# Optimization experiments

Hardware: AMD Instinct MI355X
Metric: run time of the kernel (lower is better)

Reference implementation:

```python
import jax, jax.numpy as jnp
from jax import lax
import numpy as np

B, DIM, HEADS, L, K = 8, 128, 8, 4096, 3
INNER = DIM * HEADS
PAD = K // 2
EPS = 1e-5
SCALE = DIM ** -0.5


def setup_inputs() -> dict:
    key = jax.random.key(0)
    ks = jax.random.split(key, 32)

    def n(i, shape, s):
        return jax.random.normal(ks[i], shape, jnp.float32) * s

    inp = {"x": jax.random.normal(ks[0], (B, DIM, L), jnp.float32)}
    inp["ln1_g"] = jnp.ones((DIM,), jnp.float32)
    inp["ln1_b"] = jnp.zeros((DIM,), jnp.float32)
    for idx, p in enumerate(("q", "k", "v")):
        base = 1 + idx * 2
        inp[p + "_dw"] = n(base, (DIM, 1, K), 0.2)        # depthwise kernel
        inp[p + "_bn_g"] = jnp.ones((DIM,), jnp.float32)
        inp[p + "_bn_b"] = jnp.zeros((DIM,), jnp.float32)
        inp[p + "_bn_m"] = jnp.zeros((DIM,), jnp.float32)  # running mean
        inp[p + "_bn_v"] = jnp.ones((DIM,), jnp.float32)   # running var
        inp[p + "_pw"] = n(base + 1, (INNER, DIM), 0.05)   # 1x1 conv dim->inner
    inp["dwc_dw"] = n(8, (DIM,), 0.2)                      # kernel-1 depthwise = per-channel scale
    inp["dwc_bn_g"] = jnp.ones((DIM,), jnp.float32)
    inp["dwc_bn_b"] = jnp.zeros((DIM,), jnp.float32)
    inp["dwc_bn_m"] = jnp.zeros((DIM,), jnp.float32)
    inp["dwc_bn_v"] = jnp.ones((DIM,), jnp.float32)
    inp["dwc_pw"] = n(9, (DIM, DIM), 0.05)
    inp["out_w"] = n(10, (DIM, INNER), 0.05)
    inp["out_b"] = jnp.zeros((DIM,), jnp.float32)
    inp["ln2_g"] = jnp.ones((DIM,), jnp.float32)
    inp["ln2_b"] = jnp.zeros((DIM,), jnp.float32)
    inp["ff_w1"] = n(11, (4 * DIM, DIM), 0.05)
    inp["ff_b1"] = jnp.zeros((4 * DIM,), jnp.float32)
    inp["ff_w2"] = n(12, (DIM, 4 * DIM), 0.05)
    inp["ff_b2"] = jnp.zeros((DIM,), jnp.float32)
    return inp


def _layernorm(x, g, b):
    # channel-wise LN over axis=1 (unbiased=False variance)
    m = jnp.mean(x, axis=1, keepdims=True)
    v = jnp.var(x, axis=1, keepdims=True)
    return (x - m) / jnp.sqrt(v + EPS) * g[None, :, None] + b[None, :, None]


def _dw_block(x, dw, g, b, m, v, pw):
    # depthwise conv (k=K, same padding) -> eval-mode BN -> 1x1 conv
    y = lax.conv_general_dilated(x, dw, (1,), [(PAD, PAD)],
                                 feature_group_count=DIM,
                                 dimension_numbers=("NCH", "OIH", "NCH"))
    y = (y - m[None, :, None]) * (g / jnp.sqrt(v + EPS))[None, :, None] + b[None, :, None]
    return jnp.einsum("oi,bil->bol", pw, y)


def reference(x, ln1_g, ln1_b,
              q_dw, q_bn_g, q_bn_b, q_bn_m, q_bn_v, q_pw,
              k_dw, k_bn_g, k_bn_b, k_bn_m, k_bn_v, k_pw,
              v_dw, v_bn_g, v_bn_b, v_bn_m, v_bn_v, v_pw,
              dwc_dw, dwc_bn_g, dwc_bn_b, dwc_bn_m, dwc_bn_v, dwc_pw,
              out_w, out_b, ln2_g, ln2_b, ff_w1, ff_b1, ff_w2, ff_b2):
    # ---- attention block (PreNorm + residual) ----
    xn = _layernorm(x, ln1_g, ln1_b)
    q = _dw_block(xn, q_dw, q_bn_g, q_bn_b, q_bn_m, q_bn_v, q_pw)  # [B, INNER, L]
    k = _dw_block(xn, k_dw, k_bn_g, k_bn_b, k_bn_m, k_bn_v, k_pw)
    v = _dw_block(xn, v_dw, v_bn_g, v_bn_b, v_bn_m, v_bn_v, v_pw)

    def split(t):  # b (h d) x -> (b h) x d
        return t.reshape(B, HEADS, DIM, L).transpose(0, 1, 3, 2).reshape(B * HEADS, L, DIM)

    q, k, v = split(q), split(k), split(v)
    k_soft = jax.nn.softmax(k, axis=-1)                       # softmax over feature dim d
    kk = jnp.einsum("nxd,nxe->nde", q, k_soft) * SCALE        # [(bh), d, d]
    # DWConv gate on q (kernel-1 depthwise -> BN -> 1x1), channels = DIM
    g_ = q * dwc_dw[None, None, :]
    g_ = (g_ - dwc_bn_m) * (dwc_bn_g / jnp.sqrt(dwc_bn_v + EPS)) + dwc_bn_b
    g_ = jnp.einsum("od,nxd->nxo", dwc_pw, g_)
    gate = jax.nn.sigmoid(g_) * v
    out = jnp.einsum("nxd,nde->nxe", v, kk) + gate            # [(bh), L, d]
    out = out.reshape(B, HEADS, L, DIM).transpose(0, 1, 3, 2).reshape(B, INNER, L)
    attn = jnp.einsum("oi,bil->bol", out_w, out) + out_b[None, :, None]
    x = attn + x

    # ---- feed-forward block (PreNorm + residual) ----
    xn = _layernorm(x, ln2_g, ln2_b)
    h = jnp.einsum("oi,bil->bol", ff_w1, xn) + ff_b1[None, :, None]
    h = jax.nn.gelu(h, approximate=False)
    h = jnp.einsum("oi,bil->bol", ff_w2, h) + ff_b2[None, :, None]
    return h + x
```

## Files before the change

### kernel.cpp

```cpp
#include <hip/hip_runtime.h>
#include <hip/hip_bf16.h>
#include <math.h>

#define DI __device__ __forceinline__

namespace {

constexpr int L = 4096;
constexpr float EPS = 1e-5f;
constexpr float SCALEF = 0.08838834764831845f;

typedef unsigned short u16;
typedef unsigned int u32;
typedef unsigned char u8;
typedef __attribute__((ext_vector_type(8))) short bf16x8;
typedef __attribute__((ext_vector_type(4))) float f32x4;

DI float b2f(u16 h){ u32 u = ((u32)h) << 16; float f; __builtin_memcpy(&f, &u, 4); return f; }
DI u16 f2b(float f){ u32 u; __builtin_memcpy(&u, &f, 4); u32 r = u + 0x7fffu + ((u >> 16) & 1u); return (u16)(r >> 16); }
DI float sigmoidf(float x){ return 1.f / (1.f + __expf(-x)); }

DI uint2 pack_fp8x8(const float* v){
  u32 lo = __builtin_amdgcn_cvt_pk_fp8_f32(v[0], v[1], 0, false);
  lo = (u32)__builtin_amdgcn_cvt_pk_fp8_f32(v[2], v[3], lo, true);
  u32 hi = __builtin_amdgcn_cvt_pk_fp8_f32(v[4], v[5], 0, false);
  hi = (u32)__builtin_amdgcn_cvt_pk_fp8_f32(v[6], v[7], hi, true);
  return make_uint2(lo, hi);
}
DI u8 f2e(float v){ return (u8)__builtin_amdgcn_cvt_pk_fp8_f32(v, v, 0, false); }
DI float e2f(u8 c){ return __builtin_amdgcn_cvt_f32_fp8((int)c, 0); }

DI int boff(int o, int d8){ return ((o >> 4) << 11) + (d8 << 7) + (((o & 15) ^ d8) << 3); }
DI int foff(int g, int k8, int nn){ return (g << 11) + (k8 << 7) + (nn << 3); }
DI int faddr(int x, int e){ return ((x >> 4) << 11) + ((e >> 3) << 7) + ((x & 15) << 3) + (e & 7); }
DI int t8off(int dhi, int nl, int x8){ return (dhi << 11) + (x8 << 7) + (((nl ^ x8 ^ dhi) & 15) << 3); }

DI void stage_a(const u16* __restrict__ g, int rs, u16* a_s, int tid){
  #pragma unroll
  for (int it = 0; it < 4; it++){
    int item = tid + 256 * it;
    int d8 = item & 15, l = item >> 4;
    *(uint4*)&a_s[l * 136 + d8 * 8] = *(const uint4*)&g[(size_t)l * rs + d8 * 8];
  }
}

__global__ __launch_bounds__(256) void ln_kernel(
    const float* __restrict__ x, const float* __restrict__ g,
    const float* __restrict__ bt, u16* __restrict__ o)
{
  const int tid = threadIdx.x;
  const int pos = blockIdx.x * 64 + (tid >> 2);
  const int part = tid & 3;
  const int b = pos >> 12, l = pos & (L - 1);
  const float* xb = x + (size_t)b * 128 * L + l;
  float vv[32];
  float s = 0.f, ss = 0.f;
  #pragma unroll
  for (int i = 0; i < 32; i++){
    float v = xb[(size_t)(part * 32 + i) * L];
    vv[i] = v; s += v; ss += v * v;
  }
  s += __shfl_xor(s, 1);  s += __shfl_xor(s, 2);
  ss += __shfl_xor(ss, 1); ss += __shfl_xor(ss, 2);
  const float m = s * (1.f / 128.f);
  const float rs = rsqrtf(ss * (1.f / 128.f) - m * m + EPS);
  #pragma unroll
  for (int c = 0; c < 4; c++){
    u16 pk[8];
    #pragma unroll
    for (int j = 0; j < 8; j++){
      int d = part * 32 + c * 8 + j;
      pk[j] = f2b((vv[c * 8 + j] - m) * rs * g[d] + bt[d]);
    }
    uint4 uu; __builtin_memcpy(&uu, pk, 16);
    *(uint4*)&o[(size_t)pos * 128 + part * 32 + c * 8] = uu;
  }
}

__global__ __launch_bounds__(256) void wpack_kernel(
    const float* __restrict__ q_pw, const float* __restrict__ k_pw,
    const float* __restrict__ v_pw, const float* __restrict__ out_w,
    const float* __restrict__ ff_w1, const float* __restrict__ ff_w2,
    const float* __restrict__ dwc_dw, const float* __restrict__ dwc_bng,
    const float* __restrict__ dwc_bnv, const float* __restrict__ dwc_bnb,
    const float* __restrict__ dwc_bnm, const float* __restrict__ dwc_pw,
    u16* __restrict__ wpk, float* __restrict__ c2, u8* __restrict__ wpk8)
{
  const int blk = blockIdx.x;
  const int tid = threadIdx.x;
  if (blk < 37){
    int t8 = blk;
    #pragma unroll
    for (int it = 0; it < 8; it++){
      int item = tid + 256 * it;
      int nn = item & 15, k8 = (item >> 4) & 15, os = item >> 8;
      int o = os * 16 + nn;
      float fv[8];
      if (t8 < 24){
        int p = t8 >> 3, h = t8 & 7;
        const float* pw = (p == 0) ? q_pw : (p == 1 ? k_pw : v_pw);
        #pragma unroll
        for (int j = 0; j < 8; j++)
          fv[j] = pw[(size_t)(h * 128 + o) * 128 + k8 * 8 + j] * 16.f;
      } else if (t8 < 32){
        #pragma unroll
        for (int j = 0; j < 8; j++)
          fv[j] = out_w[(size_t)o * 1024 + (t8 - 24) * 128 + k8 * 8 + j] * 16.f;
      } else if (t8 < 36){
        #pragma unroll
        for (int j = 0; j < 8; j++)
          fv[j] = ff_w1[(size_t)((t8 - 32) * 128 + o) * 128 + k8 * 8 + j] * 16.f;
      } else {
        #pragma unroll
        for (int j = 0; j < 8; j++){
          int d = k8 * 8 + j;
          float sD = dwc_bng[d] * rsqrtf(dwc_bnv[d] + EPS);
          fv[j] = dwc_pw[(size_t)o * 128 + d] * dwc_dw[d] * sD * 16.f;
        }
      }
      *(uint2*)&wpk8[(size_t)t8 * 16384 + foff(os, k8, nn)] = pack_fp8x8(fv);
    }
  } else if (blk < 69){
    int vitem = (blk - 37) * 256 + tid;
    int d8 = vitem & 15;
    int o  = (vitem >> 4) & 127;
    int t  = 36 + (vitem >> 11);
    const float* src = ff_w2 + (size_t)o * 512 + (t - 36) * 128 + d8 * 8;
    u16 pk[8];
    #pragma unroll
    for (int j = 0; j < 8; j++) pk[j] = f2b(src[j]);
    uint4 uu; __builtin_memcpy(&uu, pk, 16);
    *(uint4*)&wpk[(size_t)t * 16384 + boff(o, d8)] = uu;
  } else {
    int e = tid;
    if (e < 128){
      float cacc = 0.f;
      for (int d = 0; d < 128; d++){
        float sD = dwc_bng[d] * rsqrtf(dwc_bnv[d] + EPS);
        cacc += dwc_pw[(size_t)e * 128 + d] * (dwc_bnb[d] - dwc_bnm[d] * sD);
      }
      c2[e] = cacc;
    }
  }
}

struct QkvArgs {
  const float* dw[3];
  const float* bng[3];
  const float* bnb[3];
  const float* bnm[3];
  const float* bnv[3];
  u8* outp[3];
};

__global__ __launch_bounds__(256, 5) void qkv_fused_kernel(
    const u16* __restrict__ xnb, const u8* __restrict__ wpk8, QkvArgs args)
{
  __shared__ __attribute__((aligned(16))) u8 y_s8[64 * 136];
  __shared__ __attribute__((aligned(16))) u8 w_s8[16384];
  __shared__ float4 coef[128];
  const int tid = threadIdx.x;
  const int lb = blockIdx.x;
  const int bz = blockIdx.y;
  const int b  = bz / 3;
  const int p  = bz % 3;
  const int l0 = lb * 64;
  const int lane = tid & 63, wv = tid >> 6;
  const int nn = lane & 15, quad = lane >> 4;
  const int d8s = tid & 15;

  if (tid < 128){
    int d = tid;
    float sD = args.bng[p][d] * rsqrtf(args.bnv[p][d] + EPS);
    const float* dw = args.dw[p];
    coef[d] = make_float4(dw[d * 3] * sD, dw[d * 3 + 1] * sD, dw[d * 3 + 2] * sD,
                          args.bnb[p][d] - args.bnm[p][d] * sD);
  }
  __syncthreads();
  float4 cf[8];
  #pragma unroll
  for (int jj = 0; jj < 8; jj++) cf[jj] = coef[d8s * 8 + jj];
  #pragma unroll
  for (int it = 0; it < 4; it++){
    int l = (tid >> 4) + it * 16;
    int gl = l0 + l;
    const u16* rowp = xnb + ((size_t)b * L + gl) * 128 + d8s * 8;
    uint4 uc = *(const uint4*)rowp;
    uint4 um = (gl > 0)     ? *(const uint4*)(rowp - 128) : make_uint4(0, 0, 0, 0);
    uint4 up = (gl < L - 1) ? *(const uint4*)(rowp + 128) : make_uint4(0, 0, 0, 0);
    u16 em[8], ec[8], ep[8];
    __builtin_memcpy(em, &um, 16); __builtin_memcpy(ec, &uc, 16); __builtin_memcpy(ep, &up, 16);
    float fv[8];
    #pragma unroll
    for (int jj = 0; jj < 8; jj++)
      fv[jj] = cf[jj].x * b2f(em[jj]) + cf[jj].y * b2f(ec[jj]) + cf[jj].z * b2f(ep[jj]) + cf[jj].w;
    *(uint2*)&y_s8[l * 136 + d8s * 8] = pack_fp8x8(fv);
  }
  __syncthreads();
  long afq[4];
  #pragma unroll
  for (int dc = 0; dc < 4; dc++)
    afq[dc] = *(const long*)&y_s8[(wv * 16 + nn) * 136 + ((dc << 2) + quad) * 8];

  for (int h = 0; h < 8; h++){
    if (h) __syncthreads();
    const u8* src = wpk8 + ((size_t)(p * 8 + h) << 14);
    #pragma unroll
    for (int it = 0; it < 4; it++){
      int idx = (tid + 256 * it) << 4;
      *(uint4*)&w_s8[idx] = *(const uint4*)&src[idx];
    }
    __syncthreads();
    f32x4 acc[8];
    #pragma unroll
    for (int os = 0; os < 8; os++) acc[os] = (f32x4){0.f, 0.f, 0.f, 0.f};
    #pragma unroll
    for (int os = 0; os < 8; os++){
      #pragma unroll
      for (int dc = 0; dc < 4; dc++){
        int d8 = (dc << 2) + quad;
        long bf8 = *(const long*)&w_s8[foff(os, d8, nn)];
        acc[os] = __builtin_amdgcn_mfma_f32_16x16x32_fp8_fp8(afq[dc], bf8, acc[os], 0, 0, 0);
      }
    }
    #pragma unroll
    for (int os = 0; os < 8; os++)
      #pragma unroll
      for (int r = 0; r < 4; r++) acc[os][r] *= 0.0625f;
    if (p == 1){
      #pragma unroll
      for (int r = 0; r < 4; r++){
        float m = acc[0][r];
        #pragma unroll
        for (int os = 1; os < 8; os++) m = fmaxf(m, acc[os][r]);
        m = fmaxf(m, __shfl_xor(m, 1));
        m = fmaxf(m, __shfl_xor(m, 2));
        m = fmaxf(m, __shfl_xor(m, 4));
        m = fmaxf(m, __shfl_xor(m, 8));
        float s = 0.f;
        #pragma unroll
        for (int os = 0; os < 8; os++){ acc[os][r] = __expf(acc[os][r] - m); s += acc[os][r]; }
        s += __shfl_xor(s, 1);
        s += __shfl_xor(s, 2);
        s += __shfl_xor(s, 4);
        s += __shfl_xor(s, 8);
        float inv = 16.f / s;
        #pragma unroll
        for (int os = 0; os < 8; os++) acc[os][r] *= inv;
      }
    }
    __syncthreads();
    u8* st8 = w_s8;
    if (p == 2){
      #pragma unroll
      for (int os = 0; os < 8; os++){
        int e = (os << 4) + nn;
        #pragma unroll
        for (int r = 0; r < 4; r++)
          st8[faddr(wv * 16 + quad * 4 + r, e)] = f2e(acc[os][r]);
      }
    } else {
      #pragma unroll
      for (int os = 0; os < 8; os++){
        int e = (os << 4) + nn;
        #pragma unroll
        for (int r = 0; r < 4; r++)
          st8[(wv * 16 + quad * 4 + r) * 136 + e] = f2e(acc[os][r]);
      }
    }
    __syncthreads();
    if (p == 2){
      u8* v8 = args.outp[2];
      size_t tbase = ((size_t)((b * 8 + h) * 64 + lb)) << 13;
      #pragma unroll
      for (int it = 0; it < 2; it++){
        int idx = (tid + 256 * it) << 4;
        *(uint4*)&v8[tbase + idx] = *(const uint4*)&st8[idx];
      }
    } else {
      u8* outp8 = args.outp[p];
      size_t gbase = ((size_t)(b * 8 + h) * L + l0) * 128;
      #pragma unroll
      for (int it = 0; it < 4; it++){
        int item = tid + 256 * it;
        int row = item >> 4, d8 = item & 15;
        *(uint2*)&outp8[gbase + (size_t)row * 128 + d8 * 8] =
            *(const uint2*)&st8[row * 136 + d8 * 8];
      }
    }
  }
}

__global__ __launch_bounds__(256, 3) void kk_kernel(
    const u8* __restrict__ qt8, const u8* __restrict__ kt8,
    float* __restrict__ kkp)
{
  __shared__ u8 qT8[16384];
  __shared__ u8 kT8[16384];
  const int tid = threadIdx.x;
  const int sp = blockIdx.x;
  const int n  = blockIdx.y;
  const int d8 = tid & 15;
  const int x8 = tid >> 4;
  const int lane = tid & 63, wv = tid >> 6;
  const int nn = lane & 15, quad = lane >> 4;
  const int m4 = (wv >> 1) << 2;
  const int e4 = (wv & 1) << 2;
  const size_t gbase = ((size_t)n * L + sp * 1024) * 128;

  uint2 rq[8], rk[8];
  #pragma unroll
  for (int j = 0; j < 8; j++){
    size_t off = gbase + (size_t)(x8 * 8 + j) * 128 + d8 * 8;
    rq[j] = *(const uint2*)&qt8[off];
    rk[j] = *(const uint2*)&kt8[off];
  }

  f32x4 acc[4][4];
  #pragma unroll
  for (int mi = 0; mi < 4; mi++)
    #pragma unroll
    for (int ei = 0; ei < 4; ei++) acc[mi][ei] = (f32x4){0.f, 0.f, 0.f, 0.f};

  for (int c = 0; c < 8; c++){
    #pragma unroll
    for (int i = 0; i < 8; i++){
      u8 cq[8], ck[8];
      #pragma unroll
      for (int j = 0; j < 8; j++){
        u8 tmp[8];
        __builtin_memcpy(tmp, &rq[j], 8); cq[j] = tmp[i];
        __builtin_memcpy(tmp, &rk[j], 8); ck[j] = tmp[i];
      }
      int d = d8 * 8 + i;
      int off = t8off(d >> 4, d & 15, x8);
      uint2 uq, uk;
      __builtin_memcpy(&uq, cq, 8); __builtin_memcpy(&uk, ck, 8);
      *(uint2*)&qT8[off] = uq;
      *(uint2*)&kT8[off] = uk;
    }
    __syncthreads();
    if (c < 7){
      #pragma unroll
      for (int j = 0; j < 8; j++){
        size_t off = gbase + (size_t)((c + 1) * 128 + x8 * 8 + j) * 128 + d8 * 8;
        rq[j] = *(const uint2*)&qt8[off];
        rk[j] = *(const uint2*)&kt8[off];
      }
    }
    #pragma unroll
    for (int ks = 0; ks < 4; ks++){
      int x8f = (ks << 2) + quad;
      long af[4], bf[4];
      #pragma unroll
      for (int t = 0; t < 4; t++){
        af[t] = *(const long*)&qT8[t8off(m4 + t, nn, x8f)];
        bf[t] = *(const long*)&kT8[t8off(e4 + t, nn, x8f)];
      }
      #pragma unroll
      for (int mi = 0; mi < 4; mi++)
        #pragma unroll
        for (int ei = 0; ei < 4; ei++)
          acc[mi][ei] = __builtin_amdgcn_mfma_f32_16x16x32_fp8_fp8(af[mi], bf[ei], acc[mi][ei], 0, 0, 0);
    }
    __syncthreads();
  }

  float* op = kkp + ((size_t)(sp * 64 + n) << 14);
  #pragma unroll
  for (int mi = 0; mi < 4; mi++){
    #pragma unroll
    for (int r = 0; r < 4; r++){
      int d = (m4 << 4) + mi * 16 + quad * 4 + r;
      #pragma unroll
      for (int ei = 0; ei < 4; ei++)
        op[d * 128 + (e4 << 4) + ei * 16 + nn] = acc[mi][ei][r];
    }
  }
}

__global__ __launch_bounds__(256) void kkred_kernel(
    const float* __restrict__ kkp, u8* __restrict__ kkbb8)
{
  int item = blockIdx.x * 256 + threadIdx.x;
  int nn = item & 15, d8 = (item >> 4) & 15, os = (item >> 8) & 7, n = item >> 11;
  int e = os * 16 + nn;
  float fv[8];
  #pragma unroll
  for (int j = 0; j < 8; j++){
    float s = 0.f;
    #pragma unroll
    for (int sp = 0; sp < 4; sp++)
      s += kkp[(size_t)sp * (64 * 16384) + n * 16384 + (d8 * 8 + j) * 128 + e];
    fv[j] = s * (SCALEF * 2.f);
  }
  *(uint2*)&kkbb8[((size_t)n << 14) + foff(os, d8, nn)] = pack_fp8x8(fv);
}

__global__ __launch_bounds__(256, 4) void gateout_kernel(
    const u8* __restrict__ qt8, const u8* __restrict__ vt8,
    const u8* __restrict__ kkbb8, const u8* __restrict__ w2tb8,
    const float* __restrict__ c2, u8* __restrict__ outt8)
{
  __shared__ __attribute__((aligned(16))) u8 q_s8[64 * 144];
  __shared__ __attribute__((aligned(16))) u8 v_s8[8192];
  const int tid = threadIdx.x;
  const int lb = blockIdx.x;
  const int n  = blockIdx.y;
  const int l0 = lb * 64;
  const int lane = tid & 63, wv = tid >> 6;
  const int nn = lane & 15, quad = lane >> 4;
  const size_t vtile = ((size_t)(n * 64 + lb)) << 13;
  const size_t qbase = ((size_t)n * L + l0) * 128;

  #pragma unroll
  for (int it = 0; it < 4; it++){
    int item = tid + 256 * it;
    int d8b = item & 15, l = item >> 4;
    *(uint2*)&q_s8[l * 144 + d8b * 8] = *(const uint2*)&qt8[qbase + (size_t)l * 128 + d8b * 8];
  }
  #pragma unroll
  for (int it = 0; it < 2; it++){
    int idx = (tid + 256 * it) << 4;
    *(uint4*)&v_s8[idx] = *(const uint4*)&vt8[vtile + idx];
  }
  __syncthreads();

  long aq[4], av[4];
  #pragma unroll
  for (int dc = 0; dc < 4; dc++){
    aq[dc] = *(const long*)&q_s8[(wv * 16 + nn) * 144 + ((dc << 2) + quad) * 8];
    av[dc] = *(const long*)&v_s8[foff(wv, (dc << 2) + quad, nn)];
  }
  const u8* kb8 = kkbb8 + ((size_t)n << 14);
  f32x4 acc_o[8], acc_g[8];
  #pragma unroll
  for (int os = 0; os < 8; os++){ acc_o[os] = (f32x4){0,0,0,0}; acc_g[os] = (f32x4){0,0,0,0}; }
  #pragma unroll
  for (int os = 0; os < 8; os++){
    #pragma unroll
    for (int dc = 0; dc < 4; dc++){
      int d8 = (dc << 2) + quad;
      long bkk = *(const long*)&kb8[foff(os, d8, nn)];
      long bw8 = *(const long*)&w2tb8[foff(os, d8, nn)];
      acc_o[os] = __builtin_amdgcn_mfma_f32_16x16x32_fp8_fp8(av[dc], bkk, acc_o[os], 0, 0, 0);
      acc_g[os] = __builtin_amdgcn_mfma_f32_16x16x32_fp8_fp8(aq[dc], bw8, acc_g[os], 0, 0, 0);
    }
  }
  __syncthreads();
  u8* st8 = q_s8;
  #pragma unroll
  for (int os = 0; os < 8; os++){
    int e = (os << 4) + nn;
    float c2v = c2[e];
    #pragma unroll
    for (int r = 0; r < 4; r++){
      int xr = wv * 16 + quad * 4 + r;
      float ve = e2f(v_s8[faddr(xr, e)]);
      float val = acc_o[os][r] * (1.f / 32.f) + sigmoidf(acc_g[os][r] * 0.0625f + c2v) * ve;
      st8[faddr(xr, e)] = f2e(val);
    }
  }
  __syncthreads();
  #pragma unroll
  for (int it = 0; it < 2; it++){
    int idx = (tid + 256 * it) << 4;
    *(uint4*)&outt8[vtile + idx] = *(const uint4*)&st8[idx];
  }
}

__global__ __launch_bounds__(256, 4) void outw_kernel(
    const u8* __restrict__ outt8, const u8* __restrict__ wpk8o,
    const float* __restrict__ out_b, const float* __restrict__ x,
    const float* __restrict__ g2, const float* __restrict__ bt2,
    float* __restrict__ x2, u8* __restrict__ xn2b8)
{
  __shared__ float stf[128 * 68];
  const int tid = threadIdx.x;
  const int lb = blockIdx.x;
  const int b  = blockIdx.y;
  const int l0 = lb * 64;
  const int lane = tid & 63, wv = tid >> 6;
  const int nn = lane & 15, quad = lane >> 4;
  f32x4 acc[8];
  #pragma unroll
  for (int os = 0; os < 8; os++) acc[os] = (f32x4){0,0,0,0};

  for (int h = 0; h < 8; h++){
    const size_t tbase = ((size_t)((b * 8 + h) * 64 + lb)) << 13;
    long af[4];
    #pragma unroll
    for (int dc = 0; dc < 4; dc++)
      af[dc] = *(const long*)&outt8[tbase + foff(wv, (dc << 2) + quad, nn)];
    const u8* bp8 = wpk8o + (h << 14);
    #pragma unroll
    for (int os = 0; os < 8; os++){
      #pragma unroll
      for (int dc = 0; dc < 4; dc++){
        long bf8 = *(const long*)&bp8[foff(os, (dc << 2) + quad, nn)];
        acc[os] = __builtin_amdgcn_mfma_f32_16x16x32_fp8_fp8(af[dc], bf8, acc[os], 0, 0, 0);
      }
    }
  }
  #pragma unroll
  for (int os = 0; os < 8; os++)
    #pragma unroll
    for (int r = 0; r < 4; r++)
      stf[((os << 4) + nn) * 68 + wv * 16 + quad * 4 + r] = acc[os][r] * 0.0625f;
  __syncthreads();
  {
    int o = tid >> 1, lh = tid & 1;
    float bias = out_b[o];
    size_t gbase = ((size_t)b * 128 + o) * L + l0 + lh * 32;
    float* sp = &stf[o * 68 + lh * 32];
    #pragma unroll
    for (int k = 0; k < 8; k++){
      float4 xv = *(const float4*)&x[gbase + k * 4];
      float4 sv = *(float4*)&sp[k * 4];
      float4 ov = make_float4(sv.x + bias + xv.x, sv.y + bias + xv.y,
                              sv.z + bias + xv.z, sv.w + bias + xv.w);
      *(float4*)&sp[k * 4] = ov;
      *(float4*)&x2[gbase + k * 4] = ov;
    }
  }
  __syncthreads();
  {
    int l = tid >> 2, part = tid & 3;
    float vv[32];
    float s = 0.f, ss = 0.f;
    #pragma unroll
    for (int i = 0; i < 32; i++){
      float v = stf[(part * 32 + i) * 68 + l];
      vv[i] = v; s += v; ss += v * v;
    }
    s += __shfl_xor(s, 1);  s += __shfl_xor(s, 2);
    ss += __shfl_xor(ss, 1); ss += __shfl_xor(ss, 2);
    float m = s * (1.f / 128.f);
    float rs = rsqrtf(ss * (1.f / 128.f) - m * m + EPS);
    #pragma unroll
    for (int c = 0; c < 4; c++){
      float fv[8];
      #pragma unroll
      for (int j = 0; j < 8; j++){
        int d = part * 32 + c * 8 + j;
        fv[j] = (vv[c * 8 + j] - m) * rs * g2[d] + bt2[d];
      }
      *(uint2*)&xn2b8[((size_t)b * L + l0 + l) * 128 + part * 32 + c * 8] = pack_fp8x8(fv);
    }
  }
}

__global__ __launch_bounds__(256, 4) void ff_fused_kernel(
    const u8* __restrict__ xn2b8, const u8* __restrict__ wpk8,
    const u16* __restrict__ wpk,
    const float* __restrict__ b1, const float* __restrict__ b2,
    const float* __restrict__ x2, float* __restrict__ outp)
{
  __shared__ __attribute__((aligned(16))) u8 a_s8[64 * 136];
  __shared__ u16 h_s[64 * 136];
  const int tid = threadIdx.x;
  const int lb = blockIdx.x;
  const int b  = blockIdx.y;
  const int l0 = lb * 64;
  const int lane = tid & 63, wv = tid >> 6;
  const int nn = lane & 15, quad = lane >> 4;

  #pragma unroll
  for (int it = 0; it < 4; it++){
    int item = tid + 256 * it;
    int d8 = item & 15, l = item >> 4;
    *(uint2*)&a_s8[l * 136 + d8 * 8] =
        *(const uint2*)&xn2b8[((size_t)b * L + l0 + l) * 128 + d8 * 8];
  }
  __syncthreads();
  long af8[4];
  #pragma unroll
  for (int dc = 0; dc < 4; dc++)
    af8[dc] = *(const long*)&a_s8[(wv * 16 + nn) * 136 + ((dc << 2) + quad) * 8];

  f32x4 acc_out[8];
  #pragma unroll
  for (int os = 0; os < 8; os++) acc_out[os] = (f32x4){0.f, 0.f, 0.f, 0.f};

  for (int fc = 0; fc < 4; fc++){
    const u8* bp1 = wpk8 + (size_t)(32 + fc) * 16384;
    f32x4 hacc[8];
    #pragma unroll
    for (int os = 0; os < 8; os++) hacc[os] = (f32x4){0.f, 0.f, 0.f, 0.f};
    #pragma unroll
    for (int os = 0; os < 8; os++){
      #pragma unroll
      for (int dc = 0; dc < 4; dc++){
        long bf8 = *(const long*)&bp1[foff(os, (dc << 2) + quad, nn)];
        hacc[os] = __builtin_amdgcn_mfma_f32_16x16x32_fp8_fp8(af8[dc], bf8, hacc[os], 0, 0, 0);
      }
    }
    __syncthreads();
    #pragma unroll
    for (int os = 0; os < 8; os++){
      float bias = b1[fc * 128 + (os << 4) + nn];
      #pragma unroll
      for (int r = 0; r < 4; r++){
        float v = hacc[os][r] * 0.0625f + bias;
        float ge = 0.5f * v * (1.f + erff(v * 0.70710678118654752f));
        h_s[(wv * 16 + quad * 4 + r) * 136 + (os << 4) + nn] = f2b(ge);
      }
    }
    __syncthreads();
    bf16x8 hf[4];
    #pragma unroll
    for (int dc = 0; dc < 4; dc++)
      hf[dc] = *(const bf16x8*)&h_s[(wv * 16 + nn) * 136 + ((dc << 2) + quad) * 8];
    const u16* bp2 = wpk + (size_t)(36 + fc) * 16384;
    #pragma unroll
    for (int os = 0; os < 8; os++){
      #pragma unroll
      for (int dc = 0; dc < 4; dc++){
        int d8 = (dc << 2) + quad;
        bf16x8 bf = *(const bf16x8*)&bp2[(os << 11) + (d8 << 7) + ((nn ^ d8) << 3)];
        acc_out[os] = __builtin_amdgcn_mfma_f32_16x16x32_bf16(hf[dc], bf, acc_out[os], 0, 0, 0);
      }
    }
  }

  float* stf = (float*)h_s;
  #pragma unroll
  for (int t = 0; t < 2; t++){
    __syncthreads();
    #pragma unroll
    for (int osl = 0; osl < 4; osl++){
      int os = t * 4 + osl;
      #pragma unroll
      for (int r = 0; r < 4; r++)
        stf[((osl << 4) + nn) * 68 + wv * 16 + quad * 4 + r] = acc_out[os][r];
    }
    __syncthreads();
    int ol = tid >> 2;
    int o  = t * 64 + ol;
    int lc = (tid & 3) * 16;
    float bias = b2[o];
    size_t gbase = ((size_t)b * 128 + o) * L + l0 + lc;
    #pragma unroll
    for (int k = 0; k < 4; k++){
      float4 sv = *(const float4*)&stf[ol * 68 + lc + k * 4];
      float4 xv = *(const float4*)&x2[gbase + k * 4];
      *(float4*)&outp[gbase + k * 4] = make_float4(sv.x + bias + xv.x, sv.y + bias + xv.y,
                                                   sv.z + bias + xv.z, sv.w + bias + xv.w);
    }
  }
}

}

extern "C" void kernel_launch(void* const* d_in, const int* in_sizes, int n_in,
                              void* d_out, int out_size, void* d_ws, size_t ws_size,
                              hipStream_t stream)
{
  const float* x      = (const float*)d_in[0];
  const float* ln1_g  = (const float*)d_in[1];
  const float* ln1_b  = (const float*)d_in[2];
  const float* q_dw   = (const float*)d_in[3];
  const float* q_bng  = (const float*)d_in[4];
  const float* q_bnb  = (const float*)d_in[5];
  const float* q_bnm  = (const float*)d_in[6];
  const float* q_bnv  = (const float*)d_in[7];
  const float* q_pw   = (const float*)d_in[8];
  const float* k_dw   = (const float*)d_in[9];
  const float* k_bng  = (const float*)d_in[10];
  const float* k_bnb  = (const float*)d_in[11];
  const float* k_bnm  = (const float*)d_in[12];
  const float* k_bnv  = (const float*)d_in[13];
  const float* k_pw   = (const float*)d_in[14];
  const float* v_dw   = (const float*)d_in[15];
  const float* v_bng  = (const float*)d_in[16];
  const float* v_bnb  = (const float*)d_in[17];
  const float* v_bnm  = (const float*)d_in[18];
  const float* v_bnv  = (const float*)d_in[19];
  const float* v_pw   = (const float*)d_in[20];
  const float* dwc_dw  = (const float*)d_in[21];
  const float* dwc_bng = (const float*)d_in[22];
  const float* dwc_bnb = (const float*)d_in[23];
  const float* dwc_bnm = (const float*)d_in[24];
  const float* dwc_bnv = (const float*)d_in[25];
  const float* dwc_pw  = (const float*)d_in[26];
  const float* out_w  = (const float*)d_in[27];
  const float* out_b  = (const float*)d_in[28];
  const float* ln2_g  = (const float*)d_in[29];
  const float* ln2_b  = (const float*)d_in[30];
  const float* ff_w1  = (const float*)d_in[31];
  const float* ff_b1  = (const float*)d_in[32];
  const float* ff_w2  = (const float*)d_in[33];
  const float* ff_b2  = (const float*)d_in[34];
  float* out = (float*)d_out;

  char* w = (char*)d_ws;
  u8*   qt8   = (u8*)(w);
  u8*   kt8   = (u8*)(w + (32ull  << 20));
  u8*   outt8 = (u8*)(w + (64ull  << 20));
  u8*   vt8   = (u8*)(w + (128ull << 20));
  u16*  xnb   = (u16*)(w + (192ull << 20));
  u8*   kkbb8 = (u8*)(w + (192ull << 20));
  u8*   xn2b8 = (u8*)(w + (192ull << 20));
  float* kkp  = (float*)(w + (200ull << 20));
  float* x2   = kkp;
  float* c2   = (float*)(w + (216ull << 20));
  u16*  wpk   = (u16*)(w + (216ull << 20) + 65536);
  u8*   wpk8  = (u8*)(w + (218ull << 20));
  u8*   wpk8o = wpk8 + ((size_t)24 << 14);
  u8*   w2tb8 = wpk8 + ((size_t)36 << 14);

  ln_kernel<<<512, 256, 0, stream>>>(x, ln1_g, ln1_b, xnb);
  wpack_kernel<<<70, 256, 0, stream>>>(q_pw, k_pw, v_pw, out_w, ff_w1, ff_w2,
                                       dwc_dw, dwc_bng, dwc_bnv, dwc_bnb, dwc_bnm, dwc_pw,
                                       wpk, c2, wpk8);

  QkvArgs qa;
  qa.dw[0] = q_dw;  qa.bng[0] = q_bng; qa.bnb[0] = q_bnb; qa.bnm[0] = q_bnm; qa.bnv[0] = q_bnv; qa.outp[0] = qt8;
  qa.dw[1] = k_dw;  qa.bng[1] = k_bng; qa.bnb[1] = k_bnb; qa.bnm[1] = k_bnm; qa.bnv[1] = k_bnv; qa.outp[1] = kt8;
  qa.dw[2] = v_dw;  qa.bng[2] = v_bng; qa.bnb[2] = v_bnb; qa.bnm[2] = v_bnm; qa.bnv[2] = v_bnv; qa.outp[2] = vt8;
  qkv_fused_kernel<<<dim3(64, 24), 256, 0, stream>>>(xnb, wpk8, qa);

  kk_kernel<<<dim3(4, 64), 256, 0, stream>>>(qt8, kt8, kkp);
  kkred_kernel<<<512, 256, 0, stream>>>(kkp, kkbb8);
  gateout_kernel<<<dim3(64, 64), 256, 0, stream>>>(qt8, vt8, kkbb8, w2tb8, c2, outt8);
  outw_kernel<<<dim3(64, 8), 256, 0, stream>>>(outt8, wpk8o, out_b, x, ln2_g, ln2_b, x2, xn2b8);

  ff_fused_kernel<<<dim3(64, 8), 256, 0, stream>>>(xn2b8, wpk8, wpk, ff_b1, ff_b2, x2, out);
}
```

Before: 354.7 us.

## Fuse LN1 with weight packing and fuse out-projection with feed-forward block

Merges the LayerNorm-1 kernel and the weight-packing kernel into a single prep launch selected by block index. Fuses the attention output projection, residual, LayerNorm-2 and the feed-forward block into one kernel, keeping x2 and the normalized fp8 activations in shared memory instead of writing and rereading them from global memory. This removes two launches and a global round trip of the intermediate tensors. The cost is more shared memory per block, which lowers the occupancy bound from 4 to 3 blocks per CU.

Result: slower. 419.7 us (+18.3%).

```diff
diff --git a/kernel.cpp b/kernel.cpp
--- a/kernel.cpp
+++ b/kernel.cpp
@@ -35,49 +35,9 @@
 DI int faddr(int x, int e){ return ((x >> 4) << 11) + ((e >> 3) << 7) + ((x & 15) << 3) + (e & 7); }
 DI int t8off(int dhi, int nl, int x8){ return (dhi << 11) + (x8 << 7) + (((nl ^ x8 ^ dhi) & 15) << 3); }
 
-DI void stage_a(const u16* __restrict__ g, int rs, u16* a_s, int tid){
-  #pragma unroll
-  for (int it = 0; it < 4; it++){
-    int item = tid + 256 * it;
-    int d8 = item & 15, l = item >> 4;
-    *(uint4*)&a_s[l * 136 + d8 * 8] = *(const uint4*)&g[(size_t)l * rs + d8 * 8];
-  }
-}
-
-__global__ __launch_bounds__(256) void ln_kernel(
-    const float* __restrict__ x, const float* __restrict__ g,
-    const float* __restrict__ bt, u16* __restrict__ o)
-{
-  const int tid = threadIdx.x;
-  const int pos = blockIdx.x * 64 + (tid >> 2);
-  const int part = tid & 3;
-  const int b = pos >> 12, l = pos & (L - 1);
-  const float* xb = x + (size_t)b * 128 * L + l;
-  float vv[32];
-  float s = 0.f, ss = 0.f;
-  #pragma unroll
-  for (int i = 0; i < 32; i++){
-    float v = xb[(size_t)(part * 32 + i) * L];
-    vv[i] = v; s += v; ss += v * v;
-  }
-  s += __shfl_xor(s, 1);  s += __shfl_xor(s, 2);
-  ss += __shfl_xor(ss, 1); ss += __shfl_xor(ss, 2);
-  const float m = s * (1.f / 128.f);
-  const float rs = rsqrtf(ss * (1.f / 128.f) - m * m + EPS);
-  #pragma unroll
-  for (int c = 0; c < 4; c++){
-    u16 pk[8];
-    #pragma unroll
-    for (int j = 0; j < 8; j++){
-      int d = part * 32 + c * 8 + j;
-      pk[j] = f2b((vv[c * 8 + j] - m) * rs * g[d] + bt[d]);
-    }
-    uint4 uu; __builtin_memcpy(&uu, pk, 16);
-    *(uint4*)&o[(size_t)pos * 128 + part * 32 + c * 8] = uu;
-  }
-}
-
-__global__ __launch_bounds__(256) void wpack_kernel(
+__global__ __launch_bounds__(256) void prep_kernel(
+    const float* __restrict__ x, const float* __restrict__ ln1_g,
+    const float* __restrict__ ln1_b, u16* __restrict__ xnb,
     const float* __restrict__ q_pw, const float* __restrict__ k_pw,
     const float* __restrict__ v_pw, const float* __restrict__ out_w,
     const float* __restrict__ ff_w1, const float* __restrict__ ff_w2,
@@ -86,8 +46,37 @@
     const float* __restrict__ dwc_bnm, const float* __restrict__ dwc_pw,
     u16* __restrict__ wpk, float* __restrict__ c2, u8* __restrict__ wpk8)
 {
-  const int blk = blockIdx.x;
   const int tid = threadIdx.x;
+  if (blockIdx.x < 512){
+    const int pos = blockIdx.x * 64 + (tid >> 2);
+    const int part = tid & 3;
+    const int b = pos >> 12, l = pos & (L - 1);
+    const float* xb = x + (size_t)b * 128 * L + l;
+    float vv[32];
+    float s = 0.f, ss = 0.f;
+    #pragma unroll
+    for (int i = 0; i < 32; i++){
+      float v = xb[(size_t)(part * 32 + i) * L];
+      vv[i] = v; s += v; ss += v * v;
+    }
+    s += __shfl_xor(s, 1);  s += __shfl_xor(s, 2);
+    ss += __shfl_xor(ss, 1); ss += __shfl_xor(ss, 2);
+    const float m = s * (1.f / 128.f);
+    const float rs = rsqrtf(ss * (1.f / 128.f) - m * m + EPS);
+    #pragma unroll
+    for (int c = 0; c < 4; c++){
+      u16 pk[8];
+      #pragma unroll
+      for (int j = 0; j < 8; j++){
+        int d = part * 32 + c * 8 + j;
+        pk[j] = f2b((vv[c * 8 + j] - m) * rs * ln1_g[d] + ln1_b[d]);
+      }
+      uint4 uu; __builtin_memcpy(&uu, pk, 16);
+      *(uint4*)&xnb[(size_t)pos * 128 + part * 32 + c * 8] = uu;
+    }
+    return;
+  }
+  const int blk = blockIdx.x - 512;
   if (blk < 37){
     int t8 = blk;
     #pragma unroll
@@ -469,44 +458,53 @@
   }
 }
 
-__global__ __launch_bounds__(256, 4) void outw_kernel(
-    const u8* __restrict__ outt8, const u8* __restrict__ wpk8o,
+__global__ __launch_bounds__(256, 3) void attn_ff_kernel(
+    const u8* __restrict__ outt8, const u8* __restrict__ wpk8,
+    const u16* __restrict__ wpk,
     const float* __restrict__ out_b, const float* __restrict__ x,
     const float* __restrict__ g2, const float* __restrict__ bt2,
-    float* __restrict__ x2, u8* __restrict__ xn2b8)
+    const float* __restrict__ b1, const float* __restrict__ b2,
+    float* __restrict__ outp)
 {
   __shared__ float stf[128 * 68];
+  __shared__ __attribute__((aligned(16))) u16 hs_u[64 * 136];
+  u8* a_s8 = (u8*)hs_u;
+  u16* h_s = hs_u;
+  float* stf2 = (float*)hs_u;
   const int tid = threadIdx.x;
   const int lb = blockIdx.x;
   const int b  = blockIdx.y;
   const int l0 = lb * 64;
   const int lane = tid & 63, wv = tid >> 6;
   const int nn = lane & 15, quad = lane >> 4;
-  f32x4 acc[8];
-  #pragma unroll
-  for (int os = 0; os < 8; os++) acc[os] = (f32x4){0,0,0,0};
-
-  for (int h = 0; h < 8; h++){
-    const size_t tbase = ((size_t)((b * 8 + h) * 64 + lb)) << 13;
-    long af[4];
-    #pragma unroll
-    for (int dc = 0; dc < 4; dc++)
-      af[dc] = *(const long*)&outt8[tbase + foff(wv, (dc << 2) + quad, nn)];
-    const u8* bp8 = wpk8o + (h << 14);
-    #pragma unroll
-    for (int os = 0; os < 8; os++){
-      #pragma unroll
-      for (int dc = 0; dc < 4; dc++){
-        long bf8 = *(const long*)&bp8[foff(os, (dc << 2) + quad, nn)];
-        acc[os] = __builtin_amdgcn_mfma_f32_16x16x32_fp8_fp8(af[dc], bf8, acc[os], 0, 0, 0);
-      }
-    }
-  }
-  #pragma unroll
-  for (int os = 0; os < 8; os++)
-    #pragma unroll
-    for (int r = 0; r < 4; r++)
-      stf[((os << 4) + nn) * 68 + wv * 16 + quad * 4 + r] = acc[os][r] * 0.0625f;
+
+  {
+    f32x4 acc[8];
+    #pragma unroll
+    for (int os = 0; os < 8; os++) acc[os] = (f32x4){0,0,0,0};
+    const u8* wpk8o = wpk8 + ((size_t)24 << 14);
+    for (int h = 0; h < 8; h++){
+      const size_t tbase = ((size_t)((b * 8 + h) * 64 + lb)) << 13;
+      long af[4];
+      #pragma unroll
+      for (int dc = 0; dc < 4; dc++)
+        af[dc] = *(const long*)&outt8[tbase + foff(wv, (dc << 2) + quad, nn)];
+      const u8* bp8 = wpk8o + (h << 14);
+      #pragma unroll
+      for (int os = 0; os < 8; os++){
+        #pragma unroll
+        for (int dc = 0; dc < 4; dc++){
+          long bf8 = *(const long*)&bp8[foff(os, (dc << 2) + quad, nn)];
+          acc[os] = __builtin_amdgcn_mfma_f32_16x16x32_fp8_fp8(af[dc], bf8, acc[os], 0, 0, 0);
+        }
+      }
+    }
+    #pragma unroll
+    for (int os = 0; os < 8; os++)
+      #pragma unroll
+      for (int r = 0; r < 4; r++)
+        stf[((os << 4) + nn) * 68 + wv * 16 + quad * 4 + r] = acc[os][r] * 0.0625f;
+  }
   __syncthreads();
   {
     int o = tid >> 1, lh = tid & 1;
@@ -517,10 +515,8 @@
     for (int k = 0; k < 8; k++){
       float4 xv = *(const float4*)&x[gbase + k * 4];
       float4 sv = *(float4*)&sp[k * 4];
-      float4 ov = make_float4(sv.x + bias + xv.x, sv.y + bias + xv.y,
-                              sv.z + bias + xv.z, sv.w + bias + xv.w);
-      *(float4*)&sp[k * 4] = ov;
-      *(float4*)&x2[gbase + k * 4] = ov;
+      *(float4*)&sp[k * 4] = make_float4(sv.x + bias + xv.x, sv.y + bias + xv.y,
+                                         sv.z + bias + xv.z, sv.w + bias + xv.w);
     }
   }
   __syncthreads();
@@ -545,32 +541,8 @@
         int d = part * 32 + c * 8 + j;
         fv[j] = (vv[c * 8 + j] - m) * rs * g2[d] + bt2[d];
       }
-      *(uint2*)&xn2b8[((size_t)b * L + l0 + l) * 128 + part * 32 + c * 8] = pack_fp8x8(fv);
-    }
-  }
-}
-
-__global__ __launch_bounds__(256, 4) void ff_fused_kernel(
-    const u8* __restrict__ xn2b8, const u8* __restrict__ wpk8,
-    const u16* __restrict__ wpk,
-    const float* __restrict__ b1, const float* __restrict__ b2,
-    const float* __restrict__ x2, float* __restrict__ outp)
-{
-  __shared__ __attribute__((aligned(16))) u8 a_s8[64 * 136];
-  __shared__ u16 h_s[64 * 136];
-  const int tid = threadIdx.x;
-  const int lb = blockIdx.x;
-  const int b  = blockIdx.y;
-  const int l0 = lb * 64;
-  const int lane = tid & 63, wv = tid >> 6;
-  const int nn = lane & 15, quad = lane >> 4;
-
-  #pragma unroll
-  for (int it = 0; it < 4; it++){
-    int item = tid + 256 * it;
-    int d8 = item & 15, l = item >> 4;
-    *(uint2*)&a_s8[l * 136 + d8 * 8] =
-        *(const uint2*)&xn2b8[((size_t)b * L + l0 + l) * 128 + d8 * 8];
+      *(uint2*)&a_s8[l * 136 + part * 32 + c * 8] = pack_fp8x8(fv);
+    }
   }
   __syncthreads();
   long af8[4];
@@ -623,7 +595,6 @@
     }
   }
 
-  float* stf = (float*)h_s;
   #pragma unroll
   for (int t = 0; t < 2; t++){
     __syncthreads();
@@ -632,7 +603,7 @@
       int os = t * 4 + osl;
       #pragma unroll
       for (int r = 0; r < 4; r++)
-        stf[((osl << 4) + nn) * 68 + wv * 16 + quad * 4 + r] = acc_out[os][r];
+        stf2[((osl << 4) + nn) * 68 + wv * 16 + quad * 4 + r] = acc_out[os][r];
     }
     __syncthreads();
     int ol = tid >> 2;
@@ -642,8 +613,8 @@
     size_t gbase = ((size_t)b * 128 + o) * L + l0 + lc;
     #pragma unroll
     for (int k = 0; k < 4; k++){
-      float4 sv = *(const float4*)&stf[ol * 68 + lc + k * 4];
-      float4 xv = *(const float4*)&x2[gbase + k * 4];
+      float4 sv = *(const float4*)&stf2[ol * 68 + lc + k * 4];
+      float4 xv = *(const float4*)&stf[o * 68 + lc + k * 4];
       *(float4*)&outp[gbase + k * 4] = make_float4(sv.x + bias + xv.x, sv.y + bias + xv.y,
                                                    sv.z + bias + xv.z, sv.w + bias + xv.w);
     }
@@ -700,17 +671,14 @@
   u8*   vt8   = (u8*)(w + (128ull << 20));
   u16*  xnb   = (u16*)(w + (192ull << 20));
   u8*   kkbb8 = (u8*)(w + (192ull << 20));
-  u8*   xn2b8 = (u8*)(w + (192ull << 20));
   float* kkp  = (float*)(w + (200ull << 20));
-  float* x2   = kkp;
   float* c2   = (float*)(w + (216ull << 20));
   u16*  wpk   = (u16*)(w + (216ull << 20) + 65536);
   u8*   wpk8  = (u8*)(w + (218ull << 20));
-  u8*   wpk8o = wpk8 + ((size_t)24 << 14);
   u8*   w2tb8 = wpk8 + ((size_t)36 << 14);
 
-  ln_kernel<<<512, 256, 0, stream>>>(x, ln1_g, ln1_b, xnb);
-  wpack_kernel<<<70, 256, 0, stream>>>(q_pw, k_pw, v_pw, out_w, ff_w1, ff_w2,
+  prep_kernel<<<582, 256, 0, stream>>>(x, ln1_g, ln1_b, xnb,
+                                       q_pw, k_pw, v_pw, out_w, ff_w1, ff_w2,
                                        dwc_dw, dwc_bng, dwc_bnv, dwc_bnb, dwc_bnm, dwc_pw,
                                        wpk, c2, wpk8);
 
@@ -723,7 +691,6 @@
   kk_kernel<<<dim3(4, 64), 256, 0, stream>>>(qt8, kt8, kkp);
   kkred_kernel<<<512, 256, 0, stream>>>(kkp, kkbb8);
   gateout_kernel<<<dim3(64, 64), 256, 0, stream>>>(qt8, vt8, kkbb8, w2tb8, c2, outt8);
-  outw_kernel<<<dim3(64, 8), 256, 0, stream>>>(outt8, wpk8o, out_b, x, ln2_g, ln2_b, x2, xn2b8);
-
-  ff_fused_kernel<<<dim3(64, 8), 256, 0, stream>>>(xn2b8, wpk8, wpk, ff_b1, ff_b2, x2, out);
-}
+  attn_ff_kernel<<<dim3(64, 8), 256, 0, stream>>>(outt8, wpk8, wpk, out_b, x,
+                                                  ln2_g, ln2_b, ff_b1, ff_b2, out);
+}
```
